# Kernel tuning notes

Measured on AMD Instinct MI355X. Metric: run time of the kernel, lower is better.

## Reference

```python
import jax, jax.numpy as jnp
import numpy as np
import math

# Config (mirrors KoopmanConfig)
B = 4096          # batch
C = 128           # context_dim
D = 32            # latent_dim
K = 8             # num_experts
R = 8             # low_rank
NSEG = 3
STEPS = [8, 8, 8] # steps_per_segment, sums to HORIZON
HORIZON = 24
DT = 0.1
DECAY_TARGET = 0.7
DECAY_SCALE = 1.0
SIGMA_MAX = 1.0
MAX_FROB = 3.0
TEMP = 2.0        # gate_temperature_start (stage 1)
EPS = 1e-6


def expm_fixed(M):
    """Matrix exponential via scaling-and-squaring + Taylor (Horner).
    Valid because ||M*dt|| is small (A Frobenius-clamped to 3, Q diag <= 1, dt=0.1).
    Fully differentiable and batched over leading dims."""
    SQ = 6       # scale by 2^-6 -> norm ~0.01
    ORDER = 14
    A = M / (2.0 ** SQ)
    n = M.shape[-1]
    I = jnp.eye(n, dtype=M.dtype)
    Rm = I
    for k in range(ORDER, 0, -1):
        Rm = I + (A @ Rm) / k
    for _ in range(SQ):
        Rm = Rm @ Rm
    return Rm


def setup_inputs() -> dict:
    key = jax.random.key(0)
    ks = jax.random.split(key, 10)
    def init(k, shape, fan_in):
        return jax.random.normal(k, shape, jnp.float32) / np.float32(np.sqrt(fan_in))
    return {
        "context": jax.random.normal(ks[0], (B, C), jnp.float32),
        "z0": jax.random.normal(ks[1], (B, D), jnp.float32),
        # per-segment stacked Linear params (torch Linear: y = x @ W + b)
        "S_W": init(ks[2], (NSEG, C, K * D * D), C),
        "S_b": jnp.zeros((NSEG, K * D * D), jnp.float32),
        "L_W": init(ks[3], (NSEG, C, K * D * R), C),
        "L_b": jnp.zeros((NSEG, K * D * R), jnp.float32),
        "G_W": init(ks[4], (NSEG, C, K), C),
        "G_b": jnp.zeros((NSEG, K), jnp.float32),
        "Sig_W": init(ks[5], (NSEG, C, D), C),
        "Sig_b": jnp.zeros((NSEG, D), jnp.float32),
    }


def reference(context, z0, S_W, S_b, L_W, L_b, G_W, G_b, Sig_W, Sig_b):
    b = context.shape[0]
    mu = jnp.float32(-math.log(DECAY_TARGET) / (DT * HORIZON) * DECAY_SCALE)
    I = jnp.eye(D, dtype=context.dtype)
    z = z0
    cov = jnp.zeros((b, D, D), context.dtype)
    states_all, covs_all = [], []
    for s in range(NSEG):
        # SegmentExpertGenerator
        raw_S = (context @ S_W[s] + S_b[s]).reshape(b, K, D, D)
        skew = raw_S - jnp.swapaxes(raw_S, -1, -2)
        raw_L = (context @ L_W[s] + L_b[s]).reshape(b, K, D, R)
        LLT = jnp.einsum('bkdr,bker->bkde', raw_L, raw_L)
        A_experts = skew - LLT - mu * I                      # [b,K,D,D]
        logits = context @ G_W[s] + G_b[s]
        w = jax.nn.softmax(logits / max(TEMP, EPS), axis=-1)  # [b,K]
        A = jnp.einsum('bk,bkde->bde', w, A_experts)
        # clamp_frobenius
        frob = jnp.linalg.norm(A.reshape(b, -1), axis=-1)
        scale = jnp.where(frob > MAX_FROB, MAX_FROB / (frob + EPS), jnp.float32(1.0))
        A = A * scale[:, None, None]
        # SigmaGenerator: diagonal Sigma -> Q = Sigma Sigma^T = diag(diag^2)
        diag = jnp.minimum(jax.nn.softplus(context @ Sig_W[s] + Sig_b[s]), SIGMA_MAX)
        Q = (diag ** 2)[:, :, None] * I                      # [b,D,D]
        # Van Loan discretization: expm([[A, Q], [0, -A^T]] * dt)
        top = jnp.concatenate([A, Q], axis=-1)
        bot = jnp.concatenate([jnp.zeros_like(Q), -jnp.swapaxes(A, -1, -2)], axis=-1)
        M = jnp.concatenate([top, bot], axis=-2)             # [b,2D,2D]
        E = expm_fixed(M * DT)
        Phi = E[..., :D, :D]
        Qd = Phi @ E[..., :D, D:]
        Qd = 0.5 * (Qd + jnp.swapaxes(Qd, -1, -2))
        PhiT = jnp.swapaxes(Phi, -1, -2)
        def step(carry, _):
            zc, cc = carry
            zc = jnp.einsum('bij,bj->bi', Phi, zc)
            cc = Phi @ cc @ PhiT + Qd
            cc = 0.5 * (cc + jnp.swapaxes(cc, -1, -2))
            return (zc, cc), (zc, cc)
        (z, cov), (zs, cs) = jax.lax.scan(step, (z, cov), None, length=STEPS[s])
        states_all.append(jnp.swapaxes(zs, 0, 1))   # [b,steps,D]
        covs_all.append(jnp.swapaxes(cs, 0, 1))     # [b,steps,D,D]
    states = jnp.concatenate(states_all, axis=1)    # [b,HORIZON,D]
    covariances = jnp.concatenate(covs_all, axis=1) # [b,HORIZON,D,D]
    return states, covariances
```

## Files before the change

### kernel.cpp

```cpp
#include <hip/hip_runtime.h>
#include <math.h>


#define NSEGC 3
#define BSZ   4096
#define MUC   0.14861455999447191f
#define XSC   0.025f
#define XRS(r) (((r) & 7) << 2)

typedef unsigned short ushort_t;
typedef unsigned int uint_t;
typedef __attribute__((ext_vector_type(8))) short bf16x8;
typedef __attribute__((ext_vector_type(16))) float f32x16;

__device__ __forceinline__ void ld4(float d[4], const float* p) {
  const float4 v = *(const float4*)p; d[0]=v.x; d[1]=v.y; d[2]=v.z; d[3]=v.w;
}
__device__ __forceinline__ void st4(float* p, const float d[4]) {
  *(float4*)p = make_float4(d[0], d[1], d[2], d[3]);
}
__device__ __forceinline__ unsigned short bf_rne(float x) {
  unsigned b = __float_as_uint(x);
  unsigned r = b + 0x7FFFu + ((b >> 16) & 1u);
  return (unsigned short)(r >> 16);
}

__global__ __launch_bounds__(64) void kA(const float* __restrict__ ctx,
    const float* __restrict__ GW, const float* __restrict__ Gb,
    const float* __restrict__ SgW, const float* __restrict__ Sgb,
    float* __restrict__ Wsm, float* __restrict__ Q2) {
  const int b = blockIdx.x, s = blockIdx.y, l = threadIdx.x;
  __shared__ float c[128];
  c[l]      = ctx[(size_t)b*128 + l];
  c[l + 64] = ctx[(size_t)b*128 + 64 + l];
  __syncthreads();
  if (l < 8) {
    float acc = Gb[s*8 + l];
    #pragma unroll 4
    for (int q = 0; q < 128; ++q) acc += c[q] * GW[(size_t)(s*128 + q)*8 + l];
    float li = acc * 0.5f;
    float m = li;
    m = fmaxf(m, __shfl_xor(m, 1));
    m = fmaxf(m, __shfl_xor(m, 2));
    m = fmaxf(m, __shfl_xor(m, 4));
    float e = expf(li - m);
    float sum = e;
    sum += __shfl_xor(sum, 1);
    sum += __shfl_xor(sum, 2);
    sum += __shfl_xor(sum, 4);
    Wsm[((size_t)s*BSZ + b)*8 + l] = e / sum;
  } else if (l < 40) {
    const int d = l - 8;
    float acc = Sgb[s*32 + d];
    #pragma unroll 4
    for (int q = 0; q < 128; ++q) acc += c[q] * SgW[(size_t)(s*128 + q)*32 + d];
    float sp = fmaxf(acc, 0.f) + log1pf(expf(-fabsf(acc)));
    float dg = fminf(sp, 1.0f);
    Q2[((size_t)s*BSZ + b)*32 + d] = dg * dg;
  }
}

__global__ __launch_bounds__(256) void kA2(const float* __restrict__ ctx,
                                           float* __restrict__ ctxT) {
  __shared__ float tile[32][33];
  const int bb = blockIdx.x * 32, cc = blockIdx.y * 32;
  const int tx = threadIdx.x & 31, ty = threadIdx.x >> 5;
  for (int r = ty; r < 32; r += 8) tile[r][tx] = ctx[(size_t)(bb + r)*128 + cc + tx];
  __syncthreads();
  for (int r = ty; r < 32; r += 8) ctxT[(size_t)(cc + r)*BSZ + bb + tx] = tile[tx][r];
}

__global__ __launch_bounds__(256) void kCvtA(const float* __restrict__ ctx,
    const float* __restrict__ Wsm, ushort_t* __restrict__ Ah,
    ushort_t* __restrict__ Al, int s) {
  __shared__ float cs[128];
  __shared__ float wwv[8];
  const int b = blockIdx.x, t = threadIdx.x;
  if (t < 128) cs[t] = ctx[(size_t)b*128 + t];
  else if (t < 136) wwv[t - 128] = Wsm[((size_t)s*BSZ + b)*8 + (t - 128)];
  __syncthreads();
  for (int kc = t; kc < 1088; kc += 256) {
    float v = 0.f;
    if (kc < 1024) v = wwv[kc >> 7] * cs[kc & 127];
    else if (kc < 1032) v = wwv[kc - 1024];
    const unsigned short h = bf_rne(v);
    const float hf = __uint_as_float(((unsigned)h) << 16);
    Ah[(size_t)b*1088 + kc] = h;
    Al[(size_t)b*1088 + kc] = bf_rne(v - hf);
  }
}

__global__ __launch_bounds__(256) void kCvtB(const float* __restrict__ SW,
    const float* __restrict__ Sb, ushort_t* __restrict__ Bh,
    ushort_t* __restrict__ Bl) {
  const int n = blockIdx.x, s = blockIdx.y, t = threadIdx.x;
  const int i = n >> 5, j = n & 31, nT = j*32 + i;
  ushort_t* bh = Bh + (size_t)s*1114112;
  ushort_t* bl = Bl + (size_t)s*1114112;
  for (int kc = t; kc < 1088; kc += 256) {
    float v = 0.f;
    if (kc < 1024) {
      const int k = kc >> 7, c = kc & 127;
      const float* base = SW + ((size_t)(s*128 + c))*8192 + (size_t)k*1024;
      v = base[n] - base[nT];
    } else if (kc < 1032) {
      const int k = kc - 1024;
      const float* base = Sb + (size_t)s*8192 + (size_t)k*1024;
      v = base[n] - base[nT];
    }
    const unsigned short h = bf_rne(v);
    const float hf = __uint_as_float(((unsigned)h) << 16);
    bh[(size_t)n*1088 + kc] = h;
    bl[(size_t)n*1088 + kc] = bf_rne(v - hf);
  }
}

__global__ __launch_bounds__(256) void kB3(const ushort_t* __restrict__ Ah,
    const ushort_t* __restrict__ Al, const ushort_t* __restrict__ Bh,
    const ushort_t* __restrict__ Bl, float* __restrict__ ASseg) {
  __shared__ ushort_t sArr[2][2][8192];
  const int t = threadIdx.x;
  const int l = t & 63, w = t >> 6;
  const int hh = l >> 5, lane31 = l & 31;
  const int nb = blockIdx.x * 128, bb = blockIdx.y * 128;
  const int wr0 = (w & 1) * 64, wc0 = (w >> 1) * 64;

  const ushort_t* APT[3] = {Ah, Ah, Al};
  const ushort_t* BPT[3] = {Bh, Bl, Bh};

  f32x16 acc[2][2];
  #pragma unroll
  for (int a = 0; a < 2; ++a)
    #pragma unroll
    for (int bq = 0; bq < 2; ++bq)
      #pragma unroll
      for (int e = 0; e < 16; ++e) acc[a][bq][e] = 0.f;

  #define STAGE(buf, it) do {                                                  \
    const int p_ = (it) / 17, ks_ = (it) - p_*17;                              \
    const ushort_t* As_ = APT[p_];                                             \
    const ushort_t* Bs_ = BPT[p_];                                             \
    _Pragma("unroll")                                                          \
    for (int i_ = 0; i_ < 4; ++i_) {                                           \
      const int gidx_ = i_*256 + t;                                            \
      const int r_ = gidx_ >> 3, g_ = gidx_ & 7;                               \
      const int gs_ = g_ ^ (r_ & 7);                                           \
      const ushort_t* srcA_ = As_ + (size_t)(bb + r_)*1088 + ks_*64 + gs_*8;   \
      const ushort_t* srcB_ = Bs_ + (size_t)(nb + r_)*1088 + ks_*64 + gs_*8;   \
      __builtin_amdgcn_global_load_lds(                                        \
        (const __attribute__((address_space(1))) unsigned int*)srcA_,          \
        (__attribute__((address_space(3))) unsigned int*)&sArr[buf][0][(i_*256 + w*64)*8], \
        16, 0, 0);                                                             \
      __builtin_amdgcn_global_load_lds(                                        \
        (const __attribute__((address_space(1))) unsigned int*)srcB_,          \
        (__attribute__((address_space(3))) unsigned int*)&sArr[buf][1][(i_*256 + w*64)*8], \
        16, 0, 0);                                                             \
    }                                                                          \
  } while (0)

  STAGE(0, 0);
  int cur = 0;
  #pragma unroll 1
  for (int it = 0; it < 51; ++it) {
    __syncthreads();
    if (it + 1 < 51) STAGE(cur ^ 1, it + 1);
    const ushort_t* lA = &sArr[cur][0][0];
    const ushort_t* lB = &sArr[cur][1][0];
    #pragma unroll
    for (int kc = 0; kc < 4; ++kc) {
      bf16x8 af[2], bfr[2];
      #pragma unroll
      for (int rt = 0; rt < 2; ++rt) {
        const int row = wr0 + rt*32 + lane31;
        const int slot = (kc*2 + hh) ^ (row & 7);
        af[rt] = *(const bf16x8*)&lA[row*64 + slot*8];
      }
      #pragma unroll
      for (int ct = 0; ct < 2; ++ct) {
        const int row = wc0 + ct*32 + lane31;
        const int slot = (kc*2 + hh) ^ (row & 7);
        bfr[ct] = *(const bf16x8*)&lB[row*64 + slot*8];
      }
      #pragma unroll
      for (int rt = 0; rt < 2; ++rt)
        #pragma unroll
        for (int ct = 0; ct < 2; ++ct)
          acc[rt][ct] = __builtin_amdgcn_mfma_f32_32x32x16_bf16(
              af[rt], bfr[ct], acc[rt][ct], 0, 0, 0);
    }
    cur ^= 1;
  }
  #undef STAGE

  #pragma unroll
  for (int rt = 0; rt < 2; ++rt)
    #pragma unroll
    for (int ct = 0; ct < 2; ++ct) {
      float* o = ASseg + ((size_t)(bb + wr0 + rt*32))*1024 + nb + wc0 + ct*32 + lane31;
      #pragma unroll
      for (int reg = 0; reg < 16; ++reg) {
        const int row = (reg & 3) + 8*(reg >> 2) + 4*hh;
        o[(size_t)row*1024] = acc[rt][ct][reg];
      }
    }
}

__global__ __launch_bounds__(256) void kL(const float* __restrict__ ctxT,
    const float* __restrict__ LW, const float* __restrict__ Lb,
    const float* __restrict__ Wsm, float* __restrict__ LT, int s) {
  __shared__ float At[32][128];
  __shared__ float Bt[32][128];
  __shared__ float wsq[8][128];
  const int t = threadIdx.x;
  const int nb = blockIdx.x * 128, bb = blockIdx.y * 128;
  for (int i = t; i < 1024; i += 256) {
    const int k = i >> 7, x = i & 127;
    wsq[k][x] = sqrtf(Wsm[((size_t)s*BSZ + bb + x)*8 + k]);
  }
  float acc[8][8] = {};
  const int b0 = (t >> 4) * 8, n0 = (t & 15) * 8;
  const int qrow = t >> 3, x0 = (t & 7) * 16;
  for (int c0 = 0; c0 < 128; c0 += 32) {
    __syncthreads();
    #pragma unroll
    for (int rep = 0; rep < 4; ++rep) {
      const int x = x0 + rep*4;
      *(float4*)&At[qrow][x] = *(const float4*)&ctxT[(size_t)(c0 + qrow)*BSZ + bb + x];
      *(float4*)&Bt[qrow][x] =
        *(const float4*)&LW[((size_t)(s*128 + c0 + qrow))*2048 + nb + x];
    }
    __syncthreads();
    #pragma unroll 8
    for (int q = 0; q < 32; ++q) {
      float av[8], bv[8];
      ld4(av, &At[q][b0]); ld4(av + 4, &At[q][b0 + 4]);
      ld4(bv, &Bt[q][n0]); ld4(bv + 4, &Bt[q][n0 + 4]);
      #pragma unroll
      for (int i = 0; i < 8; ++i)
        #pragma unroll
        for (int j = 0; j < 8; ++j) acc[i][j] += av[i] * bv[j];
    }
  }
  const int kidx = (nb + n0) >> 8;
  const int dcol = ((nb + n0) >> 3) & 31;
  float lbv[8];
  #pragma unroll
  for (int j = 0; j < 8; ++j) lbv[j] = Lb[(size_t)s*2048 + nb + n0 + j];
  for (int i = 0; i < 8; ++i) {
    const float wv = wsq[kidx][b0 + i];
    float* dst = LT + (size_t)(bb + b0 + i)*2048 + kidx*256 + dcol;
    #pragma unroll
    for (int j = 0; j < 8; ++j) dst[j*32] = (acc[i][j] + lbv[j]) * wv;
  }
}

__global__ __launch_bounds__(128) void kLLT(const float* __restrict__ LT,
                                            float* __restrict__ AS, int s) {
  __shared__ float L4[4][64][32];
  const int t = threadIdx.x;
  const int bbase = blockIdx.x * 4;
  {
    float* l4f = &L4[0][0][0];
    const float* src = LT + (size_t)bbase * 2048;
    for (int i = t*4; i < 8192; i += 512)
      *(float4*)&l4f[i] = *(const float4*)&src[i];
  }
  __syncthreads();
  const int b = t >> 5, u = t & 31;
  const int i0 = (u >> 2) * 4, j0 = (u & 3) * 8;
  float acc[4][8] = {};
  #pragma unroll 8
  for (int kr = 0; kr < 64; ++kr) {
    float pa[4], pb[8];
    ld4(pa, &L4[b][kr][i0]);
    ld4(pb, &L4[b][kr][j0]); ld4(pb + 4, &L4[b][kr][j0 + 4]);
    #pragma unroll
    for (int ii = 0; ii < 4; ++ii)
      #pragma unroll
      for (int jj = 0; jj < 8; ++jj) acc[ii][jj] += pa[ii] * pb[jj];
  }
  float* dst = AS + ((size_t)s*BSZ + bbase + b)*1024;
  for (int ii = 0; ii < 4; ++ii) {
    float x[8];
    ld4(x, &dst[(i0+ii)*32 + j0]); ld4(x + 4, &dst[(i0+ii)*32 + j0 + 4]);
    #pragma unroll
    for (int jj = 0; jj < 8; ++jj) x[jj] -= acc[ii][jj];
    st4(&dst[(i0+ii)*32 + j0], x); st4(&dst[(i0+ii)*32 + j0 + 4], &x[4]);
  }
}

struct Frag { bf16x8 h0, l0, h1, l1; };

__device__ __forceinline__ void cvt8(const float x[8], bf16x8& hi, bf16x8& lo) {
  uint_t h[4], l[4];
  #pragma unroll
  for (int p = 0; p < 4; ++p) {
    const uint_t b0 = __float_as_uint(x[2*p]);
    const uint_t b1 = __float_as_uint(x[2*p + 1]);
    h[p] = __builtin_amdgcn_perm(b1, b0, 0x07060302u);
    const float l0f = x[2*p]     - __uint_as_float(b0 & 0xFFFF0000u);
    const float l1f = x[2*p + 1] - __uint_as_float(b1 & 0xFFFF0000u);
    l[p] = __builtin_amdgcn_perm(__float_as_uint(l1f), __float_as_uint(l0f),
                                 0x07060302u);
  }
  hi = __builtin_bit_cast(bf16x8, make_uint4(h[0], h[1], h[2], h[3]));
  lo = __builtin_bit_cast(bf16x8, make_uint4(l[0], l[1], l[2], l[3]));
}
__device__ __forceinline__ void rd_row8(const float* M, int r, int kb, float o[8]) {
  const float* p = M + r*32;
  ld4(o,     p + ((kb)     ^ XRS(r)));
  ld4(o + 4, p + ((kb + 4) ^ XRS(r)));
}
__device__ __forceinline__ void rd_col8(const float* M, int c, int kb, float o[8]) {
  #pragma unroll
  for (int e = 0; e < 8; ++e) o[e] = M[(kb + e)*32 + (c ^ XRS(kb + e))];
}
__device__ __forceinline__ void mkfrag_row(const float* M, int r, int hoff, Frag& f) {
  float t0[8], t1[8];
  rd_row8(M, r, hoff, t0);
  rd_row8(M, r, 16 + hoff, t1);
  cvt8(t0, f.h0, f.l0);
  cvt8(t1, f.h1, f.l1);
}
__device__ __forceinline__ void mkfrag_col(const float* M, int c, int hoff, Frag& f) {
  float t0[8], t1[8];
  rd_col8(M, c, hoff, t0);
  rd_col8(M, c, 16 + hoff, t1);
  cvt8(t0, f.h0, f.l0);
  cvt8(t1, f.h1, f.l1);
}
__device__ __forceinline__ f32x16 mmacc(const Frag& A, const Frag& B, f32x16 acc) {
  acc = __builtin_amdgcn_mfma_f32_32x32x16_bf16(A.h0, B.h0, acc, 0, 0, 0);
  acc = __builtin_amdgcn_mfma_f32_32x32x16_bf16(A.h0, B.l0, acc, 0, 0, 0);
  acc = __builtin_amdgcn_mfma_f32_32x32x16_bf16(A.l0, B.h0, acc, 0, 0, 0);
  acc = __builtin_amdgcn_mfma_f32_32x32x16_bf16(A.h1, B.h1, acc, 0, 0, 0);
  acc = __builtin_amdgcn_mfma_f32_32x32x16_bf16(A.h1, B.l1, acc, 0, 0, 0);
  acc = __builtin_amdgcn_mfma_f32_32x32x16_bf16(A.l1, B.h1, acc, 0, 0, 0);
  return acc;
}
__device__ __forceinline__ f32x16 zero16() {
  f32x16 z = {0.f,0.f,0.f,0.f,0.f,0.f,0.f,0.f,0.f,0.f,0.f,0.f,0.f,0.f,0.f,0.f};
  return z;
}
__device__ __forceinline__ void st_T(float* M, int j, int ho4, const float v[16]) {
  float* p = M + j*32;
  #pragma unroll
  for (int m = 0; m < 4; ++m) st4(p + ((8*m + ho4) ^ XRS(j)), v + 4*m);
}
__device__ __forceinline__ void ld16_T(const float* M, int j, int ho4, float o[16]) {
  const float* p = M + j*32;
  #pragma unroll
  for (int m = 0; m < 4; ++m) ld4(o + 4*m, p + ((8*m + ho4) ^ XRS(j)));
}

__global__ __launch_bounds__(64) void kC9(const float* __restrict__ AS,
    const float* __restrict__ Q2, const float* __restrict__ z0,
    float* __restrict__ out) {
  __shared__ float SA[1024];
  __shared__ float S11[1024];
  __shared__ float S12[1024];
  __shared__ float S22[1024];
  __shared__ float zarr[32], qds[32];
  const int b = blockIdx.x, t = threadIdx.x;
  const int j = t & 31, hh = t >> 5;
  const int hoff = hh * 8, ho4 = hh * 4;

  if (t < 32) zarr[t] = z0[(size_t)b*32 + t];
  float covreg[16];
  #pragma unroll
  for (int r = 0; r < 16; ++r) covreg[r] = 0.f;
  __syncthreads();

  float* covout = out + 3145728 + (size_t)b*24576;
  float* stout  = out + (size_t)b*768;

  for (int s = 0; s < NSEGC; ++s) {
    if (t < 32) qds[t] = Q2[((size_t)s*BSZ + b)*32 + t] * XSC;
    const float* asb = AS + ((size_t)s*BSZ + b)*1024;
    float av[16];
    #pragma unroll
    for (int m = 0; m < 4; ++m) ld4(av + 4*m, &asb[j*32 + 16*hh + 4*m]);
    #pragma unroll
    for (int i = 0; i < 16; ++i) if (16*hh + i == j) av[i] -= MUC;
    float ssq = 0.f;
    #pragma unroll
    for (int i = 0; i < 16; ++i) ssq += av[i]*av[i];
    #pragma unroll
    for (int off = 1; off < 64; off <<= 1) ssq += __shfl_xor(ssq, off);
    const float frob = sqrtf(ssq);
    const float sc = (frob > 3.0f ? 3.0f / (frob + 1e-6f) : 1.0f) * XSC;
    #pragma unroll
    for (int i = 0; i < 16; ++i) av[i] *= sc;
    #pragma unroll
    for (int m = 0; m < 4; ++m) {
      st4(&SA[j*32 + ((16*hh + 4*m) ^ XRS(j))], av + 4*m);
      float id[4], zo[4] = {0.f, 0.f, 0.f, 0.f};
      #pragma unroll
      for (int e = 0; e < 4; ++e) id[e] = (16*hh + 4*m + e == j) ? 1.f : 0.f;
      st4(&S11[j*32 + ((16*hh + 4*m) ^ XRS(j))], id);
      st4(&S22[j*32 + ((16*hh + 4*m) ^ XRS(j))], id);
      st4(&S12[j*32 + ((16*hh + 4*m) ^ XRS(j))], zo);
    }
    __syncthreads();
    float qv[16];
    #pragma unroll
    for (int r = 0; r < 16; ++r) qv[r] = qds[(r&3) + 8*(r>>2) + ho4];
    Frag aA, aT;
    mkfrag_row(SA, j, hoff, aA);
    mkfrag_col(SA, j, hoff, aT);

    for (int k = 5; k >= 1; --k) {
      const float rk = 1.0f / (float)k;
      Frag Bf;
      float Xs[16];
      mkfrag_row(S11, j, hoff, Bf);
      f32x16 X = mmacc(aA, Bf, zero16());
      #pragma unroll
      for (int r = 0; r < 16; ++r) {
        const int row = (r&3) + 8*(r>>2) + ho4;
        Xs[r] = X[r]*rk + (row == j ? 1.f : 0.f);
      }
      st_T(S11, j, ho4, Xs);
      mkfrag_row(S12, j, hoff, Bf);
      X = mmacc(aA, Bf, zero16());
      float rv[16];
      ld16_T(S22, j, ho4, rv);
      #pragma unroll
      for (int r = 0; r < 16; ++r) Xs[r] = (X[r] + qv[r]*rv[r]) * rk;
      st_T(S12, j, ho4, Xs);
      mkfrag_row(S22, j, hoff, Bf);
      X = mmacc(aT, Bf, zero16());
      #pragma unroll
      for (int r = 0; r < 16; ++r) {
        const int row = (r&3) + 8*(r>>2) + ho4;
        Xs[r] = (row == j ? 1.f : 0.f) - X[r]*rk;
      }
      st_T(S22, j, ho4, Xs);
    }
    __syncthreads();

    {
      Frag Ac, Br;
      float Xs[16];
      mkfrag_col(S11, j, hoff, Ac);
      mkfrag_row(S11, j, hoff, Br);
      f32x16 X1 = mmacc(Ac, Br, zero16());
      #pragma unroll
      for (int r = 0; r < 16; ++r) Xs[r] = X1[r];
      st_T(S11, j, ho4, Xs);
      Frag B12; mkfrag_row(S12, j, hoff, B12);
      f32x16 X2 = mmacc(Ac, B12, zero16());
      Frag A12; mkfrag_col(S12, j, hoff, A12);
      Frag B22; mkfrag_row(S22, j, hoff, B22);
      X2 = mmacc(A12, B22, X2);
      #pragma unroll
      for (int r = 0; r < 16; ++r) Xs[r] = X2[r];
      st_T(S12, j, ho4, Xs);
      Frag A22; mkfrag_col(S22, j, hoff, A22);
      f32x16 X3 = mmacc(A22, B22, zero16());
      #pragma unroll
      for (int r = 0; r < 16; ++r) Xs[r] = X3[r];
      st_T(S22, j, ho4, Xs);
    }
    __syncthreads();
    {
      Frag Ac, Br;
      float Xs[16];
      mkfrag_col(S11, j, hoff, Ac);
      mkfrag_row(S11, j, hoff, Br);
      f32x16 X1 = mmacc(Ac, Br, zero16());
      Frag B12; mkfrag_row(S12, j, hoff, B12);
      f32x16 X2 = mmacc(Ac, B12, zero16());
      Frag A12; mkfrag_col(S12, j, hoff, A12);
      Frag B22; mkfrag_row(S22, j, hoff, B22);
      X2 = mmacc(A12, B22, X2);
      #pragma unroll
      for (int r = 0; r < 16; ++r) Xs[r] = X1[r];
      st_T(S11, j, ho4, Xs);
      #pragma unroll
      for (int r = 0; r < 16; ++r) Xs[r] = X2[r];
      st_T(S12, j, ho4, Xs);
    }
    __syncthreads();

    Frag PhiF;
    mkfrag_col(S11, j, hoff, PhiF);
    {
      Frag B12; mkfrag_row(S12, j, hoff, B12);
      f32x16 Xq = mmacc(PhiF, B12, zero16());
      float Xs[16];
      #pragma unroll
      for (int r = 0; r < 16; ++r) Xs[r] = Xq[r];
      st_T(S22, j, ho4, Xs);
      __syncthreads();
      float sym[16];
      #pragma unroll
      for (int r = 0; r < 16; ++r) {
        const int row = (r&3) + 8*(r>>2) + ho4;
        const float tv = S22[row*32 + (j ^ XRS(row))];
        sym[r] = 0.5f * (Xs[r] + tv);
      }
      __syncthreads();
      st_T(S22, j, ho4, sym);
    }
    __syncthreads();

    st_T(S12, j, ho4, covreg);
    __syncthreads();

    for (int tt = 0; tt < 8; ++tt) {
      Frag Bcov; mkfrag_row(S12, j, hoff, Bcov);
      f32x16 G = mmacc(PhiF, Bcov, zero16());
      float Gs[16];
      #pragma unroll
      for (int r = 0; r < 16; ++r) Gs[r] = G[r];
      st_T(SA, j, ho4, Gs);
      Frag AG; mkfrag_col(SA, j, hoff, AG);
      f32x16 C = mmacc(AG, PhiF, zero16());
      float qdv[16], Cs[16];
      ld16_T(S22, j, ho4, qdv);
      #pragma unroll
      for (int r = 0; r < 16; ++r) Cs[r] = C[r] + qdv[r];
      float zp = 0.f;
      #pragma unroll
      for (int e = 0; e < 16; ++e) {
        const int kr = 16*hh + e;
        zp += S11[kr*32 + (j ^ XRS(kr))] * zarr[kr];
      }
      zp += __shfl_xor(zp, 32);
      st_T(S12, j, ho4, Cs);
      #pragma unroll
      for (int r = 0; r < 16; ++r) covreg[r] = Cs[r];
      float* cb = covout + (size_t)(s*8 + tt)*1024;
      #pragma unroll
      for (int r = 0; r < 16; ++r)
        cb[((r&3) + 8*(r>>2) + ho4)*32 + j] = Cs[r];
      if (t < 32) {
        zarr[t] = zp;
        stout[(s*8 + tt)*32 + t] = zp;
      }
      __syncthreads();
    }
  }
}

extern "C" void kernel_launch(void* const* d_in, const int* in_sizes, int n_in,
                              void* d_out, int out_size, void* d_ws, size_t ws_size,
                              hipStream_t stream) {
  const float* ctx  = (const float*)d_in[0];
  const float* z0   = (const float*)d_in[1];
  const float* S_W  = (const float*)d_in[2];
  const float* S_b  = (const float*)d_in[3];
  const float* L_W  = (const float*)d_in[4];
  const float* L_b  = (const float*)d_in[5];
  const float* G_W  = (const float*)d_in[6];
  const float* G_b  = (const float*)d_in[7];
  const float* Sg_W = (const float*)d_in[8];
  const float* Sg_b = (const float*)d_in[9];
  float* out = (float*)d_out;
  float* ws  = (float*)d_ws;

  float* w_   = ws;
  float* q2   = ws + 98304;
  float* ctxT = ws + 491520;
  float* as_  = ws + 1015808;
  ushort_t* panAh  = (ushort_t*)(ws + 13598720);
  ushort_t* panAl  = panAh + 4456448;
  ushort_t* panBh3 = panAl + 4456448;
  ushort_t* panBl3 = panBh3 + 3342336;
  float* lt = ws + 13598720;

  kA   <<<dim3(4096, 3), 64,  0, stream>>>(ctx, G_W, G_b, Sg_W, Sg_b, w_, q2);
  kA2  <<<dim3(128, 4),  256, 0, stream>>>(ctx, ctxT);
  kCvtB<<<dim3(1024, 3), 256, 0, stream>>>(S_W, S_b, panBh3, panBl3);
  for (int s = 0; s < 3; ++s) {
    kCvtA<<<dim3(4096), 256, 0, stream>>>(ctx, w_, panAh, panAl, s);
    kB3  <<<dim3(8, 32), 256, 0, stream>>>(panAh, panAl,
                                           panBh3 + (size_t)s*1114112,
                                           panBl3 + (size_t)s*1114112,
                                           as_ + (size_t)s*4194304);
  }
  for (int s = 0; s < 3; ++s) {
    kL  <<<dim3(16, 32), 256, 0, stream>>>(ctxT, L_W, L_b, w_, lt, s);
    kLLT<<<dim3(1024),   128, 0, stream>>>(lt, as_, s);
  }
  kC9 <<<dim3(4096),    64, 0, stream>>>(as_, q2, z0, out);
}
```

Baseline: 630.4 us.

## Move low-rank L GEMM to split-bf16 MFMA and trim final kernel shared memory

Replaces the FP32 SIMT GEMM that builds the low-rank factors with a bf16 MFMA kernel. It emulates FP32 accuracy through a three-product hi/lo split: ctx and L_W are pre-converted to hi/lo bf16 panels, and tiles are loaded straight into LDS with global_load_lds under double buffering. The final per-batch kernel drops one 4 KB shared buffer, reading the state propagation from Phi fragments held in registers, and adds a launch-bounds occupancy hint. This adds conversion kernels and extra workspace traffic in exchange for matrix-core throughput, with a small accuracy risk from the split-bf16 scheme.

```diff
diff --git a/kernel.cpp b/kernel.cpp
--- a/kernel.cpp
+++ b/kernel.cpp
@@ -23,6 +23,9 @@
   unsigned b = __float_as_uint(x);
   unsigned r = b + 0x7FFFu + ((b >> 16) & 1u);
   return (unsigned short)(r >> 16);
+}
+__device__ __forceinline__ float bf2f(short v) {
+  return __uint_as_float(((uint_t)(unsigned short)v) << 16);
 }
 
 __global__ __launch_bounds__(64) void kA(const float* __restrict__ ctx,
@@ -60,14 +63,30 @@
   }
 }
 
-__global__ __launch_bounds__(256) void kA2(const float* __restrict__ ctx,
-                                           float* __restrict__ ctxT) {
+__global__ __launch_bounds__(256) void kCvtX(const float* __restrict__ ctx,
+    ushort_t* __restrict__ Xh, ushort_t* __restrict__ Xl) {
+  const int idx = blockIdx.x*256 + threadIdx.x;
+  const float v = ctx[idx];
+  const unsigned short h = bf_rne(v);
+  Xh[idx] = h;
+  Xl[idx] = bf_rne(v - __uint_as_float(((unsigned)h) << 16));
+}
+
+__global__ __launch_bounds__(256) void kCvtL(const float* __restrict__ LW,
+    ushort_t* __restrict__ Lh, ushort_t* __restrict__ Ll) {
   __shared__ float tile[32][33];
-  const int bb = blockIdx.x * 32, cc = blockIdx.y * 32;
+  const int nb = blockIdx.x * 32, cb = blockIdx.y * 32, s = blockIdx.z;
   const int tx = threadIdx.x & 31, ty = threadIdx.x >> 5;
-  for (int r = ty; r < 32; r += 8) tile[r][tx] = ctx[(size_t)(bb + r)*128 + cc + tx];
+  for (int r = ty; r < 32; r += 8)
+    tile[r][tx] = LW[((size_t)(s*128 + cb + r))*2048 + nb + tx];
   __syncthreads();
-  for (int r = ty; r < 32; r += 8) ctxT[(size_t)(cc + r)*BSZ + bb + tx] = tile[tx][r];
+  for (int r = ty; r < 32; r += 8) {
+    const float v = tile[tx][r];
+    const unsigned short h = bf_rne(v);
+    const size_t o = ((size_t)s*2048 + nb + r)*128 + cb + tx;
+    Lh[o] = h;
+    Ll[o] = bf_rne(v - __uint_as_float(((unsigned)h) << 16));
+  }
 }
 
 __global__ __launch_bounds__(256) void kCvtA(const float* __restrict__ ctx,
@@ -205,53 +224,103 @@
     }
 }
 
-__global__ __launch_bounds__(256) void kL(const float* __restrict__ ctxT,
-    const float* __restrict__ LW, const float* __restrict__ Lb,
-    const float* __restrict__ Wsm, float* __restrict__ LT, int s) {
-  __shared__ float At[32][128];
-  __shared__ float Bt[32][128];
-  __shared__ float wsq[8][128];
+__global__ __launch_bounds__(256) void kL3(const ushort_t* __restrict__ Xh,
+    const ushort_t* __restrict__ Xl, const ushort_t* __restrict__ Lh,
+    const ushort_t* __restrict__ Ll, const float* __restrict__ Lb,
+    const float* __restrict__ Wsm, float* __restrict__ lt, int s) {
+  __shared__ ushort_t sArr[2][2][8192];
+  __shared__ float sqw[128][8];
   const int t = threadIdx.x;
+  const int l = t & 63, w = t >> 6;
+  const int hh = l >> 5, lane31 = l & 31;
   const int nb = blockIdx.x * 128, bb = blockIdx.y * 128;
-  for (int i = t; i < 1024; i += 256) {
-    const int k = i >> 7, x = i & 127;
-    wsq[k][x] = sqrtf(Wsm[((size_t)s*BSZ + bb + x)*8 + k]);
-  }
-  float acc[8][8] = {};
-  const int b0 = (t >> 4) * 8, n0 = (t & 15) * 8;
-  const int qrow = t >> 3, x0 = (t & 7) * 16;
-  for (int c0 = 0; c0 < 128; c0 += 32) {
-    __syncthreads();
-    #pragma unroll
-    for (int rep = 0; rep < 4; ++rep) {
-      const int x = x0 + rep*4;
-      *(float4*)&At[qrow][x] = *(const float4*)&ctxT[(size_t)(c0 + qrow)*BSZ + bb + x];
-      *(float4*)&Bt[qrow][x] =
-        *(const float4*)&LW[((size_t)(s*128 + c0 + qrow))*2048 + nb + x];
-    }
-    __syncthreads();
-    #pragma unroll 8
-    for (int q = 0; q < 32; ++q) {
-      float av[8], bv[8];
-      ld4(av, &At[q][b0]); ld4(av + 4, &At[q][b0 + 4]);
-      ld4(bv, &Bt[q][n0]); ld4(bv + 4, &Bt[q][n0 + 4]);
-      #pragma unroll
-      for (int i = 0; i < 8; ++i)
+  const int wr0 = (w & 1) * 64, wc0 = (w >> 1) * 64;
+  for (int i = t; i < 1024; i += 256)
+    sqw[i >> 3][i & 7] = sqrtf(Wsm[((size_t)s*BSZ + bb + (i >> 3))*8 + (i & 7)]);
+
+  const ushort_t* APT[3] = {Xh, Xh, Xl};
+  const ushort_t* BPT[3] = {Lh + (size_t)s*262144, Ll + (size_t)s*262144,
+                            Lh + (size_t)s*262144};
+
+  f32x16 acc[2][2];
+  #pragma unroll
+  for (int a = 0; a < 2; ++a)
+    #pragma unroll
+    for (int bq = 0; bq < 2; ++bq)
+      #pragma unroll
+      for (int e = 0; e < 16; ++e) acc[a][bq][e] = 0.f;
+
+  #define STAGEL(buf, it) do {                                                 \
+    const int p_ = (it) >> 1, ks_ = (it) & 1;                                  \
+    const ushort_t* As_ = APT[p_];                                             \
+    const ushort_t* Bs_ = BPT[p_];                                             \
+    _Pragma("unroll")                                                          \
+    for (int i_ = 0; i_ < 4; ++i_) {                                           \
+      const int gidx_ = i_*256 + t;                                            \
+      const int r_ = gidx_ >> 3, g_ = gidx_ & 7;                               \
+      const int gs_ = g_ ^ (r_ & 7);                                           \
+      const ushort_t* srcA_ = As_ + (size_t)(bb + r_)*128 + ks_*64 + gs_*8;    \
+      const ushort_t* srcB_ = Bs_ + (size_t)(nb + r_)*128 + ks_*64 + gs_*8;    \
+      __builtin_amdgcn_global_load_lds(                                        \
+        (const __attribute__((address_space(1))) unsigned int*)srcA_,          \
+        (__attribute__((address_space(3))) unsigned int*)&sArr[buf][0][(i_*256 + w*64)*8], \
+        16, 0, 0);                                                             \
+      __builtin_amdgcn_global_load_lds(                                        \
+        (const __attribute__((address_space(1))) unsigned int*)srcB_,          \
+        (__attribute__((address_space(3))) unsigned int*)&sArr[buf][1][(i_*256 + w*64)*8], \
+        16, 0, 0);                                                             \
+    }                                                                          \
+  } while (0)
+
+  STAGEL(0, 0);
+  int cur = 0;
+  #pragma unroll 1
+  for (int it = 0; it < 6; ++it) {
+    __syncthreads();
+    if (it + 1 < 6) STAGEL(cur ^ 1, it + 1);
+    const ushort_t* lA = &sArr[cur][0][0];
+    const ushort_t* lB = &sArr[cur][1][0];
+    #pragma unroll
+    for (int kc = 0; kc < 4; ++kc) {
+      bf16x8 af[2], bfr[2];
+      #pragma unroll
+      for (int rt = 0; rt < 2; ++rt) {
+        const int row = wr0 + rt*32 + lane31;
+        const int slot = (kc*2 + hh) ^ (row & 7);
+        af[rt] = *(const bf16x8*)&lA[row*64 + slot*8];
+      }
+      #pragma unroll
+      for (int ct = 0; ct < 2; ++ct) {
+        const int row = wc0 + ct*32 + lane31;
+        const int slot = (kc*2 + hh) ^ (row & 7);
+        bfr[ct] = *(const bf16x8*)&lB[row*64 + slot*8];
+      }
+      #pragma unroll
+      for (int rt = 0; rt < 2; ++rt)
         #pragma unroll
-        for (int j = 0; j < 8; ++j) acc[i][j] += av[i] * bv[j];
-    }
-  }
-  const int kidx = (nb + n0) >> 8;
-  const int dcol = ((nb + n0) >> 3) & 31;
-  float lbv[8];
-  #pragma unroll
-  for (int j = 0; j < 8; ++j) lbv[j] = Lb[(size_t)s*2048 + nb + n0 + j];
-  for (int i = 0; i < 8; ++i) {
-    const float wv = wsq[kidx][b0 + i];
-    float* dst = LT + (size_t)(bb + b0 + i)*2048 + kidx*256 + dcol;
-    #pragma unroll
-    for (int j = 0; j < 8; ++j) dst[j*32] = (acc[i][j] + lbv[j]) * wv;
-  }
+        for (int ct = 0; ct < 2; ++ct)
+          acc[rt][ct] = __builtin_amdgcn_mfma_f32_32x32x16_bf16(
+              af[rt], bfr[ct], acc[rt][ct], 0, 0, 0);
+    }
+    cur ^= 1;
+  }
+  #undef STAGEL
+
+  #pragma unroll
+  for (int rt = 0; rt < 2; ++rt)
+    #pragma unroll
+    for (int ct = 0; ct < 2; ++ct) {
+      const int n = nb + wc0 + ct*32 + lane31;
+      const float lb = Lb[(size_t)s*2048 + n];
+      const int kidx = n >> 8;
+      const int ltcol = (kidx << 8) + ((n & 7) << 5) + ((n >> 3) & 31);
+      #pragma unroll
+      for (int reg = 0; reg < 16; ++reg) {
+        const int lrow = wr0 + rt*32 + (reg & 3) + 8*(reg >> 2) + 4*hh;
+        lt[(size_t)(bb + lrow)*2048 + ltcol] =
+            (acc[rt][ct][reg] + lb) * sqw[lrow][kidx];
+      }
+    }
 }
 
 __global__ __launch_bounds__(128) void kLLT(const float* __restrict__ LT,
@@ -353,10 +422,9 @@
   for (int m = 0; m < 4; ++m) ld4(o + 4*m, p + ((8*m + ho4) ^ XRS(j)));
 }
 
-__global__ __launch_bounds__(64) void kC9(const float* __restrict__ AS,
+__global__ __launch_bounds__(64, 3) void kC10(const float* __restrict__ AS,
     const float* __restrict__ Q2, const float* __restrict__ z0,
     float* __restrict__ out) {
-  __shared__ float SA[1024];
   __shared__ float S11[1024];
   __shared__ float S12[1024];
   __shared__ float S22[1024];
@@ -391,9 +459,17 @@
     const float sc = (frob > 3.0f ? 3.0f / (frob + 1e-6f) : 1.0f) * XSC;
     #pragma unroll
     for (int i = 0; i < 16; ++i) av[i] *= sc;
+    __syncthreads();
+    #pragma unroll
+    for (int m = 0; m < 4; ++m)
+      st4(&S12[j*32 + ((16*hh + 4*m) ^ XRS(j))], av + 4*m);
+    __syncthreads();
+    Frag aA, aT;
+    mkfrag_row(S12, j, hoff, aA);
+    mkfrag_col(S12, j, hoff, aT);
+    __syncthreads();
     #pragma unroll
     for (int m = 0; m < 4; ++m) {
-      st4(&SA[j*32 + ((16*hh + 4*m) ^ XRS(j))], av + 4*m);
       float id[4], zo[4] = {0.f, 0.f, 0.f, 0.f};
       #pragma unroll
       for (int e = 0; e < 4; ++e) id[e] = (16*hh + 4*m + e == j) ? 1.f : 0.f;
@@ -405,9 +481,6 @@
     float qv[16];
     #pragma unroll
     for (int r = 0; r < 16; ++r) qv[r] = qds[(r&3) + 8*(r>>2) + ho4];
-    Frag aA, aT;
-    mkfrag_row(SA, j, hoff, aA);
-    mkfrag_col(SA, j, hoff, aT);
 
     for (int k = 5; k >= 1; --k) {
       const float rk = 1.0f / (float)k;
@@ -514,8 +587,8 @@
       float Gs[16];
       #pragma unroll
       for (int r = 0; r < 16; ++r) Gs[r] = G[r];
-      st_T(SA, j, ho4, Gs);
-      Frag AG; mkfrag_col(SA, j, hoff, AG);
+      st_T(S11, j, ho4, Gs);
+      Frag AG; mkfrag_col(S11, j, hoff, AG);
       f32x16 C = mmacc(AG, PhiF, zero16());
       float qdv[16], Cs[16];
       ld16_T(S22, j, ho4, qdv);
@@ -523,9 +596,9 @@
       for (int r = 0; r < 16; ++r) Cs[r] = C[r] + qdv[r];
       float zp = 0.f;
       #pragma unroll
-      for (int e = 0; e < 16; ++e) {
-        const int kr = 16*hh + e;
-        zp += S11[kr*32 + (j ^ XRS(kr))] * zarr[kr];
+      for (int e = 0; e < 8; ++e) {
+        zp += (bf2f(PhiF.h0[e]) + bf2f(PhiF.l0[e])) * zarr[hoff + e];
+        zp += (bf2f(PhiF.h1[e]) + bf2f(PhiF.l1[e])) * zarr[16 + hoff + e];
       }
       zp += __shfl_xor(zp, 32);
       st_T(S12, j, ho4, Cs);
@@ -562,16 +635,20 @@
 
   float* w_   = ws;
   float* q2   = ws + 98304;
-  float* ctxT = ws + 491520;
   float* as_  = ws + 1015808;
   ushort_t* panAh  = (ushort_t*)(ws + 13598720);
   ushort_t* panAl  = panAh + 4456448;
   ushort_t* panBh3 = panAl + 4456448;
   ushort_t* panBl3 = panBh3 + 3342336;
   float* lt = ws + 13598720;
+  ushort_t* cxh = (ushort_t*)(ws + 21987328);
+  ushort_t* cxl = cxh + 524288;
+  ushort_t* lwh = cxl + 524288;
+  ushort_t* lwl = lwh + 786432;
 
   kA   <<<dim3(4096, 3), 64,  0, stream>>>(ctx, G_W, G_b, Sg_W, Sg_b, w_, q2);
-  kA2  <<<dim3(128, 4),  256, 0, stream>>>(ctx, ctxT);
+  kCvtX<<<dim3(2048),    256, 0, stream>>>(ctx, cxh, cxl);
+  kCvtL<<<dim3(64, 4, 3),256, 0, stream>>>(L_W, lwh, lwl);
   kCvtB<<<dim3(1024, 3), 256, 0, stream>>>(S_W, S_b, panBh3, panBl3);
   for (int s = 0; s < 3; ++s) {
     kCvtA<<<dim3(4096), 256, 0, stream>>>(ctx, w_, panAh, panAl, s);
@@ -581,8 +658,8 @@
                                            as_ + (size_t)s*4194304);
   }
   for (int s = 0; s < 3; ++s) {
-    kL  <<<dim3(16, 32), 256, 0, stream>>>(ctxT, L_W, L_b, w_, lt, s);
+    kL3 <<<dim3(16, 32), 256, 0, stream>>>(cxh, cxl, lwh, lwl, L_b, w_, lt, s);
     kLLT<<<dim3(1024),   128, 0, stream>>>(lt, as_, s);
   }
-  kC9 <<<dim3(4096),    64, 0, stream>>>(as_, q2, z0, out);
-}
+  kC10<<<dim3(4096),    64, 0, stream>>>(as_, q2, z0, out);
+}
```

Result: faster. 608.9 us (-3.4%).
